# Performance work log

Hardware: AMD Instinct MI355X
Metric: run time of the kernel (lower is better)

## Reference

```python
import jax, jax.numpy as jnp
import numpy as np

E = 1024      # embed_dim
H = 16        # num_heads
D = E // H    # head_dim
SCALING = float(D * 1.0) ** (-0.5)


def setup_inputs() -> dict:
    key = jax.random.key(0)
    ks = jax.random.split(key, 10)
    B, L, S = 4, 2048, 2048
    query = jax.random.normal(ks[0], (B, L, E), dtype=jnp.float32)
    k_in = jax.random.normal(ks[1], (B, S, E), dtype=jnp.float32)
    v_in = jax.random.normal(ks[2], (B, S, E), dtype=jnp.float32)
    attn_bias = jax.random.normal(ks[3], (L, S), dtype=jnp.float32)
    attn_mask = jax.random.normal(ks[4], (L, S), dtype=jnp.float32)
    # in_proj: Linear(E, 3E)  (xavier-uniform-ish scale), out_proj: Linear(E, E)
    lim_in = np.sqrt(6.0 / (E + 3 * E))
    Wqkv = jax.random.uniform(ks[5], (3 * E, E), minval=-lim_in, maxval=lim_in, dtype=jnp.float32)
    bqkv = jnp.zeros((3 * E,), dtype=jnp.float32)
    lim_out = np.sqrt(1.0 / E)
    Wo = jax.random.uniform(ks[6], (E, E), minval=-lim_out, maxval=lim_out, dtype=jnp.float32)
    bo = jnp.zeros((E,), dtype=jnp.float32)
    return {"query": query, "key": k_in, "value": v_in,
            "attn_bias": attn_bias, "attn_mask": attn_mask,
            "Wqkv": Wqkv, "bqkv": bqkv, "Wo": Wo, "bo": bo}


def reference(query, key, value, attn_bias, attn_mask, Wqkv, bqkv, Wo, bo):
    B, L, _ = query.shape
    S = key.shape[1]
    # fused in_proj split into q/k/v slices (q from query, k from key, v from value)
    q = query @ Wqkv[:E].T + bqkv[:E]
    k = key @ Wqkv[E:2 * E].T + bqkv[E:2 * E]
    v = value @ Wqkv[2 * E:].T + bqkv[2 * E:]
    q = q * SCALING
    # [B, L, H, D]
    q = q.reshape(B, L, H, D)
    k = k.reshape(B, S, H, D)
    v = v.reshape(B, S, H, D)
    # scores: [B, H, L, S] with additive float mask and bias (broadcast over B, H)
    scores = jnp.einsum("blhd,bshd->bhls", q, k)
    scores = scores + attn_mask[None, None] + attn_bias[None, None]
    weights = jax.nn.softmax(scores, axis=-1)  # dropout p=0.0 -> identity
    out = jnp.einsum("bhls,bshd->blhd", weights, v).reshape(B, L, E)
    return out @ Wo.T + bo
```

## Files before the change

kernel.cpp:

```cpp
#include <hip/hip_runtime.h>
#include <hip/hip_bf16.h>

#define BB 4
#define LL 2048
#define SS 2048
#define EE 1024
#define HH 16
#define DD 64
#define MM (BB * LL)
#define LOG2E 1.44269504088896340736f

typedef unsigned short u16;
typedef u16   u16x4  __attribute__((ext_vector_type(4)));
typedef u16   u16x8  __attribute__((ext_vector_type(8)));
typedef float f32x4  __attribute__((ext_vector_type(4)));
typedef __bf16 bf16x4 __attribute__((ext_vector_type(4)));
typedef __bf16 bf16x8 __attribute__((ext_vector_type(8)));

__device__ __forceinline__ u16 f2bf(float x) {
    unsigned u = __float_as_uint(x);
    u += 0x7fffu + ((u >> 16) & 1u);
    return (u16)(u >> 16);
}
__device__ __forceinline__ float bf2f(u16 b) {
    return __uint_as_float(((unsigned)b) << 16);
}

__device__ __forceinline__ void gload16(const u16* g, u16* l) {
    __builtin_amdgcn_global_load_lds(
        (const __attribute__((address_space(1))) void*)g,
        (__attribute__((address_space(3))) void*)l, 16, 0, 0);
}

__global__ __launch_bounds__(256) void f32_to_bf16_kernel(
    const float* __restrict__ in, u16* __restrict__ out)
{
    size_t idx = ((size_t)blockIdx.x * 256 + threadIdx.x) * 8;
    f32x4 a = *(const f32x4*)(in + idx);
    f32x4 b = *(const f32x4*)(in + idx + 4);
    u16x8 o;
#pragma unroll
    for (int j = 0; j < 4; j++) { o[j] = f2bf(a[j]); o[4 + j] = f2bf(b[j]); }
    *(u16x8*)(out + idx) = o;
}

__global__ __launch_bounds__(256) void combine_bias_kernel(
    const float* __restrict__ bias, const float* __restrict__ mask,
    u16* __restrict__ comb)
{
    int idx = (blockIdx.x * 256 + threadIdx.x) * 8;
    f32x4 a0 = *(const f32x4*)(bias + idx);
    f32x4 a1 = *(const f32x4*)(bias + idx + 4);
    f32x4 m0 = *(const f32x4*)(mask + idx);
    f32x4 m1 = *(const f32x4*)(mask + idx + 4);
    u16x8 o;
#pragma unroll
    for (int j = 0; j < 4; j++) {
        o[j]     = f2bf((a0[j] + m0[j]) * LOG2E);
        o[4 + j] = f2bf((a1[j] + m1[j]) * LOG2E);
    }
    *(u16x8*)(comb + idx) = o;
}

template <int ABF16, int OUTBF16, int VOUT>
__global__ __launch_bounds__(256, 2) void gemm_bt(
    const void* __restrict__ Ap, const u16* __restrict__ Bw,
    const float* __restrict__ bias, void* __restrict__ Cp,
    int M, int N, int K, float scale)
{
    __shared__ __align__(16) u16 SH[128 * 72 + 128 * 64];
    constexpr int ASTR = ABF16 ? 64 : 72;
    u16* As = SH;
    u16* Bs = SH + 128 * ASTR;
    u16* Tr = SH;

    const int tid = threadIdx.x;
    const int lane = tid & 63, wave = tid >> 6;
    const int quad = lane >> 4, ln = lane & 15;
    const int wm = (wave & 1) * 64, wn = (wave >> 1) * 64;

    const int bid = blockIdx.x;
    const int vid = (bid & 7) * 8 + ((bid >> 3) & 7) + (bid >> 6) * 64;
    const int m0 = (vid >> 3) * 128, n0 = (vid & 7) * 128;

    const int r8 = lane >> 3, c8 = lane & 7;
    const float* Af = (const float*)Ap;
    const u16*   Ab = (const u16*)Ap + (size_t)m0 * K + c8 * 8;
    const u16*   Bg = Bw + (size_t)n0 * K + c8 * 8;

    f32x4 acc[4][4];
#pragma unroll
    for (int mt = 0; mt < 4; mt++)
#pragma unroll
        for (int nt = 0; nt < 4; nt++) acc[mt][nt] = (f32x4){0.f, 0.f, 0.f, 0.f};

    f32x4 apf[8];

    auto load_a = [&](int k0) {
        if (!ABF16) {
#pragma unroll
            for (int i = 0; i < 8; i++) {
                int chunk = tid + 256 * i, row = chunk >> 4, c = chunk & 15;
                apf[i] = *(const f32x4*)(Af + (size_t)(m0 + row) * K + k0 + c * 4);
            }
        }
    };

    load_a(0);

    const int KT = K >> 6;
    for (int kt = 0; kt < KT; kt++) {
        const int k0 = kt << 6;
        __syncthreads();
#pragma unroll
        for (int i = 0; i < 4; i++) {
            int ch = i * 4 + wave;
            int row = ch * 8 + r8;
            gload16(Bg + (size_t)row * K + k0, &Bs[ch * 512]);
            if (ABF16) gload16(Ab + (size_t)row * K + k0, &As[ch * 512]);
        }
        if (!ABF16) {
#pragma unroll
            for (int i = 0; i < 8; i++) {
                int chunk = tid + 256 * i, row = chunk >> 4, c = chunk & 15;
                u16x4 o;
#pragma unroll
                for (int j = 0; j < 4; j++) o[j] = f2bf(apf[i][j]);
                *(u16x4*)(As + row * ASTR + c * 4) = o;
            }
        }
        __syncthreads();

        if (kt + 1 < KT) load_a(k0 + 64);

#pragma unroll
        for (int ks = 0; ks < 2; ks++) {
            bf16x8 af[4], bfg[4];
#pragma unroll
            for (int mt = 0; mt < 4; mt++)
                af[mt] = *(const bf16x8*)(&As[(wm + mt * 16 + ln) * ASTR + ks * 32 + quad * 8]);
#pragma unroll
            for (int nt = 0; nt < 4; nt++)
                bfg[nt] = *(const bf16x8*)(&Bs[(wn + nt * 16 + ln) * 64 + ks * 32 + quad * 8]);
#pragma unroll
            for (int mt = 0; mt < 4; mt++)
#pragma unroll
                for (int nt = 0; nt < 4; nt++)
                    acc[mt][nt] = __builtin_amdgcn_mfma_f32_16x16x32_bf16(
                        af[mt], bfg[nt], acc[mt][nt], 0, 0, 0);
        }
    }

    if (VOUT) {
        __syncthreads();
#pragma unroll
        for (int nt = 0; nt < 4; nt++) {
            int nl = wn + nt * 16 + ln;
            float bn = bias[n0 + nl];
#pragma unroll
            for (int mt = 0; mt < 4; mt++)
#pragma unroll
                for (int r = 0; r < 4; r++) {
                    int ml = wm + mt * 16 + quad * 4 + r;
                    Tr[nl * 136 + ml] = f2bf(acc[mt][nt][r] + bn);
                }
        }
        __syncthreads();
        const int bq = m0 >> 11;
        const int s0 = m0 & 2047;
#pragma unroll
        for (int i = 0; i < 8; i++) {
            int chunk = tid + 256 * i;
            int row = chunk >> 4, c = chunk & 15;
            u16x8 v = *(const u16x8*)(Tr + row * 136 + c * 8);
            int n = n0 + row;
            int h = n >> 6, d = n & 63;
            *(u16x8*)(((u16*)Cp) + ((size_t)((bq * 16 + h) * 64 + d)) * SS + s0 + c * 8) = v;
        }
    } else {
#pragma unroll
        for (int nt = 0; nt < 4; nt++) {
            int n = n0 + wn + nt * 16 + ln;
            float bn = bias[n];
#pragma unroll
            for (int mt = 0; mt < 4; mt++) {
#pragma unroll
                for (int r = 0; r < 4; r++) {
                    int m = m0 + wm + mt * 16 + quad * 4 + r;
                    float val = (acc[mt][nt][r] + bn) * scale;
                    if (OUTBF16) ((u16*)Cp)[(size_t)m * N + n] = f2bf(val);
                    else         ((float*)Cp)[(size_t)m * N + n] = val;
                }
            }
        }
    }
}

__global__ __launch_bounds__(256, 2) void attn_kernel(
    const u16* __restrict__ qb,
    const u16* __restrict__ kb,
    const u16* __restrict__ vt,
    const u16* __restrict__ comb,
    u16* __restrict__ attn)
{
    __shared__ __align__(16) u16 KPs[128 * 136];
    __shared__ __align__(16) u16 Vs[64 * 136];
    const int tid = threadIdx.x, lane = tid & 63, wave = tid >> 6;
    const int quad = lane >> 4, ln = lane & 15;

    const int bid = blockIdx.x;
    const int vid = (bid & 7) * 128 + (bid >> 3);
    const int bh = vid >> 4, b = bh >> 4, h = bh & 15;
    const int q0 = (vid & 15) * 128;
    const int qloc0 = wave * 32;

    bf16x8 qf[2][2];
#pragma unroll
    for (int qg = 0; qg < 2; qg++)
#pragma unroll
        for (int ks = 0; ks < 2; ks++)
            qf[qg][ks] = *(const bf16x8*)(qb + (size_t)(b * LL + q0 + qloc0 + 16 * qg + ln) * EE
                                          + h * 64 + ks * 32 + quad * 8);

    const u16* cb0 = comb + (size_t)(q0 + qloc0 + ln) * SS + quad * 4;
    const u16* cb1 = cb0 + (size_t)16 * SS;

    f32x4 o[4][2];
#pragma unroll
    for (int mt = 0; mt < 4; mt++) { o[mt][0] = (f32x4){0,0,0,0}; o[mt][1] = (f32x4){0,0,0,0}; }
    f32x4 ls0 = (f32x4){0,0,0,0}, ls1 = (f32x4){0,0,0,0};

    u16x8 kreg[4], vreg[4];
    auto load_kv = [&](int s0) {
#pragma unroll
        for (int i = 0; i < 4; i++) {
            int chunk = tid + 256 * i, row = chunk >> 3, c = chunk & 7;
            kreg[i] = *(const u16x8*)(kb + (size_t)(b * SS + s0 + row) * EE + h * 64 + c * 8);
        }
#pragma unroll
        for (int i = 0; i < 4; i++) {
            int chunk = tid + 256 * i, row = chunk >> 4, c = chunk & 15;
            vreg[i] = *(const u16x8*)(vt + (size_t)(bh * 64 + row) * SS + s0 + c * 8);
        }
    };
    load_kv(0);

    for (int s0 = 0; s0 < SS; s0 += 128) {
        __syncthreads();
#pragma unroll
        for (int i = 0; i < 4; i++) {
            int chunk = tid + 256 * i, row = chunk >> 3, c = chunk & 7;
            *(u16x8*)(KPs + row * 72 + c * 8) = kreg[i];
        }
#pragma unroll
        for (int i = 0; i < 4; i++) {
            int chunk = tid + 256 * i, row = chunk >> 4, c = chunk & 15;
            *(u16x8*)(Vs + row * 136 + c * 8) = vreg[i];
        }
        u16x4 bfr[8][2];
#pragma unroll
        for (int mt = 0; mt < 8; mt++) {
            bfr[mt][0] = *(const u16x4*)(cb0 + s0 + mt * 16);
            bfr[mt][1] = *(const u16x4*)(cb1 + s0 + mt * 16);
        }
        __syncthreads();

        if (s0 + 128 < SS) load_kv(s0 + 128);

        f32x4 st[8][2];
#pragma unroll
        for (int mt = 0; mt < 8; mt++)
#pragma unroll
            for (int r = 0; r < 4; r++) {
                st[mt][0][r] = bf2f(bfr[mt][0][r]);
                st[mt][1][r] = bf2f(bfr[mt][1][r]);
            }

        __builtin_amdgcn_s_setprio(1);
#pragma unroll
        for (int mt = 0; mt < 8; mt++) {
            bf16x8 a0 = *(const bf16x8*)(KPs + (mt * 16 + ln) * 72 + quad * 8);
            bf16x8 a1 = *(const bf16x8*)(KPs + (mt * 16 + ln) * 72 + 32 + quad * 8);
            st[mt][0] = __builtin_amdgcn_mfma_f32_16x16x32_bf16(a0, qf[0][0], st[mt][0], 0, 0, 0);
            st[mt][0] = __builtin_amdgcn_mfma_f32_16x16x32_bf16(a1, qf[0][1], st[mt][0], 0, 0, 0);
            st[mt][1] = __builtin_amdgcn_mfma_f32_16x16x32_bf16(a0, qf[1][0], st[mt][1], 0, 0, 0);
            st[mt][1] = __builtin_amdgcn_mfma_f32_16x16x32_bf16(a1, qf[1][1], st[mt][1], 0, 0, 0);
        }
        __builtin_amdgcn_s_setprio(0);

        bf16x4 p[8][2];
#pragma unroll
        for (int mt = 0; mt < 8; mt++)
#pragma unroll
            for (int r = 0; r < 4; r++) {
                float e0 = __builtin_amdgcn_exp2f(st[mt][0][r]);
                float e1 = __builtin_amdgcn_exp2f(st[mt][1][r]);
                ls0[r] += e0; ls1[r] += e1;
                p[mt][0][r] = (__bf16)e0;
                p[mt][1][r] = (__bf16)e1;
            }

        __syncthreads();

#pragma unroll
        for (int mt = 0; mt < 8; mt++) {
            *(bf16x4*)(KPs + (qloc0 + ln) * 136 + mt * 16 + quad * 4)      = p[mt][0];
            *(bf16x4*)(KPs + (qloc0 + 16 + ln) * 136 + mt * 16 + quad * 4) = p[mt][1];
        }

#pragma unroll
        for (int ks = 0; ks < 4; ks++) {
            bf16x8 pf0 = *(const bf16x8*)(KPs + (qloc0 + ln) * 136 + ks * 32 + quad * 8);
            bf16x8 pf1 = *(const bf16x8*)(KPs + (qloc0 + 16 + ln) * 136 + ks * 32 + quad * 8);
            __builtin_amdgcn_s_setprio(1);
#pragma unroll
            for (int mt = 0; mt < 4; mt++) {
                bf16x8 a = *(const bf16x8*)(Vs + (mt * 16 + ln) * 136 + ks * 32 + quad * 8);
                o[mt][0] = __builtin_amdgcn_mfma_f32_16x16x32_bf16(a, pf0, o[mt][0], 0, 0, 0);
                o[mt][1] = __builtin_amdgcn_mfma_f32_16x16x32_bf16(a, pf1, o[mt][1], 0, 0, 0);
            }
            __builtin_amdgcn_s_setprio(0);
        }
    }

    float lsum0 = (ls0[0] + ls0[1]) + (ls0[2] + ls0[3]);
    float lsum1 = (ls1[0] + ls1[1]) + (ls1[2] + ls1[3]);
    lsum0 += __shfl_xor(lsum0, 16); lsum0 += __shfl_xor(lsum0, 32);
    lsum1 += __shfl_xor(lsum1, 16); lsum1 += __shfl_xor(lsum1, 32);
    float inv0 = 1.f / lsum0, inv1 = 1.f / lsum1;

#pragma unroll
    for (int mt = 0; mt < 4; mt++) {
        bf16x4 p0, p1;
#pragma unroll
        for (int r = 0; r < 4; r++) {
            p0[r] = (__bf16)(o[mt][0][r] * inv0);
            p1[r] = (__bf16)(o[mt][1][r] * inv1);
        }
        *(bf16x4*)(KPs + (qloc0 + ln) * 136 + mt * 16 + quad * 4)      = p0;
        *(bf16x4*)(KPs + (qloc0 + 16 + ln) * 136 + mt * 16 + quad * 4) = p1;
    }
#pragma unroll
    for (int i = 0; i < 4; i++) {
        int j = lane + 64 * i;
        int r = j >> 3, c = j & 7;
        u16x8 v = *(const u16x8*)(KPs + (qloc0 + r) * 136 + c * 8);
        *(u16x8*)(attn + (size_t)(b * LL + q0 + qloc0 + r) * EE + h * 64 + c * 8) = v;
    }
}

extern "C" void kernel_launch(void* const* d_in, const int* in_sizes, int n_in,
                              void* d_out, int out_size, void* d_ws, size_t ws_size,
                              hipStream_t stream)
{
    (void)in_sizes; (void)n_in; (void)out_size; (void)ws_size;
    const float* query     = (const float*)d_in[0];
    const float* key       = (const float*)d_in[1];
    const float* value     = (const float*)d_in[2];
    const float* attn_bias = (const float*)d_in[3];
    const float* attn_mask = (const float*)d_in[4];
    const float* Wqkv      = (const float*)d_in[5];
    const float* bqkv      = (const float*)d_in[6];
    const float* Wo        = (const float*)d_in[7];
    const float* bo        = (const float*)d_in[8];
    float* out = (float*)d_out;

    u16* wq_bf = (u16*)d_ws;
    u16* wo_bf = wq_bf + 3 * EE * EE;
    u16* comb  = wo_bf + EE * EE;
    u16* q_bf  = comb + (size_t)LL * SS;
    u16* k_bf  = q_bf + (size_t)MM * EE;
    u16* v_bf  = k_bf + (size_t)MM * EE;
    u16* vtr   = v_bf + (size_t)MM * EE;
    u16* attnb = vtr  + (size_t)MM * EE;

    f32_to_bf16_kernel<<<3 * EE * EE / 2048, 256, 0, stream>>>(Wqkv, wq_bf);
    f32_to_bf16_kernel<<<EE * EE / 2048, 256, 0, stream>>>(Wo, wo_bf);
    combine_bias_kernel<<<(LL * SS) / 2048, 256, 0, stream>>>(attn_bias, attn_mask, comb);

    gemm_bt<0, 1, 0><<<512, 256, 0, stream>>>(query, wq_bf,               bqkv,          q_bf, MM, EE, EE, 0.125f * LOG2E);
    gemm_bt<0, 1, 0><<<512, 256, 0, stream>>>(key,   wq_bf + EE * EE,     bqkv + EE,     k_bf, MM, EE, EE, 1.f);
    gemm_bt<0, 1, 1><<<512, 256, 0, stream>>>(value, wq_bf + 2 * EE * EE, bqkv + 2 * EE, vtr,  MM, EE, EE, 1.f);

    attn_kernel<<<1024, 256, 0, stream>>>(q_bf, k_bf, vtr, comb, attnb);

    gemm_bt<1, 0, 0><<<512, 256, 0, stream>>>(attnb, wo_bf, bo, out, MM, EE, EE, 1.f);
}
```

Measured before the change: 434.1 us.

## Double-buffer GEMM shared tiles and split attention QK work by key columns per wave

```diff
diff --git a/kernel.cpp b/kernel.cpp
--- a/kernel.cpp
+++ b/kernel.cpp
@@ -68,11 +68,11 @@
     const float* __restrict__ bias, void* __restrict__ Cp,
     int M, int N, int K, float scale)
 {
-    __shared__ __align__(16) u16 SH[128 * 72 + 128 * 64];
+    __shared__ __align__(16) u16 SH[ABF16 ? (4 * 128 * 64) : (128 * 72 + 2 * 128 * 64)];
     constexpr int ASTR = ABF16 ? 64 : 72;
-    u16* As = SH;
-    u16* Bs = SH + 128 * ASTR;
-    u16* Tr = SH;
+    u16* As  = SH;
+    u16* Bs  = SH + (ABF16 ? 2 * 128 * 64 : 128 * 72);
+    u16* Tr  = SH;
 
     const int tid = threadIdx.x;
     const int lane = tid & 63, wave = tid >> 6;
@@ -105,20 +105,32 @@
             }
         }
     };
+    auto stage_b = [&](int bu, int k0) {
+#pragma unroll
+        for (int i = 0; i < 4; i++) {
+            int ch = i * 4 + wave;
+            int row = ch * 8 + r8;
+            gload16(Bg + (size_t)row * K + k0, &Bs[bu * (128 * 64) + ch * 512]);
+        }
+    };
+    auto stage_a16 = [&](int bu, int k0) {
+#pragma unroll
+        for (int i = 0; i < 4; i++) {
+            int ch = i * 4 + wave;
+            int row = ch * 8 + r8;
+            gload16(Ab + (size_t)row * K + k0, &As[bu * (128 * 64) + ch * 512]);
+        }
+    };
 
     load_a(0);
-
+    stage_b(0, 0);
+    if (ABF16) stage_a16(0, 0);
+
+    int buf = 0;
     const int KT = K >> 6;
     for (int kt = 0; kt < KT; kt++) {
         const int k0 = kt << 6;
         __syncthreads();
-#pragma unroll
-        for (int i = 0; i < 4; i++) {
-            int ch = i * 4 + wave;
-            int row = ch * 8 + r8;
-            gload16(Bg + (size_t)row * K + k0, &Bs[ch * 512]);
-            if (ABF16) gload16(Ab + (size_t)row * K + k0, &As[ch * 512]);
-        }
         if (!ABF16) {
 #pragma unroll
             for (int i = 0; i < 8; i++) {
@@ -128,20 +140,25 @@
                 for (int j = 0; j < 4; j++) o[j] = f2bf(apf[i][j]);
                 *(u16x4*)(As + row * ASTR + c * 4) = o;
             }
-        }
-        __syncthreads();
-
-        if (kt + 1 < KT) load_a(k0 + 64);
-
+            __syncthreads();
+        }
+        if (kt + 1 < KT) {
+            stage_b(buf ^ 1, k0 + 64);
+            if (ABF16) stage_a16(buf ^ 1, k0 + 64);
+            load_a(k0 + 64);
+        }
+
+        const u16* Ar = ABF16 ? &As[buf * (128 * 64)] : As;
+        const u16* Br = &Bs[buf * (128 * 64)];
 #pragma unroll
         for (int ks = 0; ks < 2; ks++) {
             bf16x8 af[4], bfg[4];
 #pragma unroll
             for (int mt = 0; mt < 4; mt++)
-                af[mt] = *(const bf16x8*)(&As[(wm + mt * 16 + ln) * ASTR + ks * 32 + quad * 8]);
+                af[mt] = *(const bf16x8*)(&Ar[(wm + mt * 16 + ln) * ASTR + ks * 32 + quad * 8]);
 #pragma unroll
             for (int nt = 0; nt < 4; nt++)
-                bfg[nt] = *(const bf16x8*)(&Bs[(wn + nt * 16 + ln) * 64 + ks * 32 + quad * 8]);
+                bfg[nt] = *(const bf16x8*)(&Br[(wn + nt * 16 + ln) * 64 + ks * 32 + quad * 8]);
 #pragma unroll
             for (int mt = 0; mt < 4; mt++)
 #pragma unroll
@@ -149,6 +166,7 @@
                     acc[mt][nt] = __builtin_amdgcn_mfma_f32_16x16x32_bf16(
                         af[mt], bfg[nt], acc[mt][nt], 0, 0, 0);
         }
+        buf ^= 1;
     }
 
     if (VOUT) {
@@ -214,21 +232,22 @@
     const int q0 = (vid & 15) * 128;
     const int qloc0 = wave * 32;
 
-    bf16x8 qf[2][2];
-#pragma unroll
-    for (int qg = 0; qg < 2; qg++)
+    bf16x8 qf[8][2];
+#pragma unroll
+    for (int qg = 0; qg < 8; qg++)
 #pragma unroll
         for (int ks = 0; ks < 2; ks++)
-            qf[qg][ks] = *(const bf16x8*)(qb + (size_t)(b * LL + q0 + qloc0 + 16 * qg + ln) * EE
+            qf[qg][ks] = *(const bf16x8*)(qb + (size_t)(b * LL + q0 + qg * 16 + ln) * EE
                                           + h * 64 + ks * 32 + quad * 8);
 
-    const u16* cb0 = comb + (size_t)(q0 + qloc0 + ln) * SS + quad * 4;
-    const u16* cb1 = cb0 + (size_t)16 * SS;
+    const u16* cbase = comb + (size_t)(q0 + ln) * SS + wave * 32 + quad * 4;
 
     f32x4 o[4][2];
 #pragma unroll
     for (int mt = 0; mt < 4; mt++) { o[mt][0] = (f32x4){0,0,0,0}; o[mt][1] = (f32x4){0,0,0,0}; }
-    f32x4 ls0 = (f32x4){0,0,0,0}, ls1 = (f32x4){0,0,0,0};
+    float ls[8];
+#pragma unroll
+    for (int qg = 0; qg < 8; qg++) ls[qg] = 0.f;
 
     u16x8 kreg[4], vreg[4];
     auto load_kv = [&](int s0) {
@@ -257,56 +276,60 @@
             int chunk = tid + 256 * i, row = chunk >> 4, c = chunk & 15;
             *(u16x8*)(Vs + row * 136 + c * 8) = vreg[i];
         }
-        u16x4 bfr[8][2];
-#pragma unroll
-        for (int mt = 0; mt < 8; mt++) {
-            bfr[mt][0] = *(const u16x4*)(cb0 + s0 + mt * 16);
-            bfr[mt][1] = *(const u16x4*)(cb1 + s0 + mt * 16);
-        }
+        u16x4 bfr[2][8];
+#pragma unroll
+        for (int m = 0; m < 2; m++)
+#pragma unroll
+            for (int qg = 0; qg < 8; qg++)
+                bfr[m][qg] = *(const u16x4*)(cbase + (size_t)qg * 16 * SS + s0 + m * 16);
         __syncthreads();
 
         if (s0 + 128 < SS) load_kv(s0 + 128);
 
-        f32x4 st[8][2];
-#pragma unroll
-        for (int mt = 0; mt < 8; mt++)
-#pragma unroll
-            for (int r = 0; r < 4; r++) {
-                st[mt][0][r] = bf2f(bfr[mt][0][r]);
-                st[mt][1][r] = bf2f(bfr[mt][1][r]);
+        f32x4 st[2][8];
+#pragma unroll
+        for (int m = 0; m < 2; m++)
+#pragma unroll
+            for (int qg = 0; qg < 8; qg++)
+#pragma unroll
+                for (int r = 0; r < 4; r++)
+                    st[m][qg][r] = bf2f(bfr[m][qg][r]);
+
+        __builtin_amdgcn_s_setprio(1);
+#pragma unroll
+        for (int m = 0; m < 2; m++) {
+            const int row = (wave * 2 + m) * 16 + ln;
+            bf16x8 a0 = *(const bf16x8*)(KPs + row * 72 + quad * 8);
+            bf16x8 a1 = *(const bf16x8*)(KPs + row * 72 + 32 + quad * 8);
+#pragma unroll
+            for (int qg = 0; qg < 8; qg++) {
+                st[m][qg] = __builtin_amdgcn_mfma_f32_16x16x32_bf16(a0, qf[qg][0], st[m][qg], 0, 0, 0);
+                st[m][qg] = __builtin_amdgcn_mfma_f32_16x16x32_bf16(a1, qf[qg][1], st[m][qg], 0, 0, 0);
             }
-
-        __builtin_amdgcn_s_setprio(1);
-#pragma unroll
-        for (int mt = 0; mt < 8; mt++) {
-            bf16x8 a0 = *(const bf16x8*)(KPs + (mt * 16 + ln) * 72 + quad * 8);
-            bf16x8 a1 = *(const bf16x8*)(KPs + (mt * 16 + ln) * 72 + 32 + quad * 8);
-            st[mt][0] = __builtin_amdgcn_mfma_f32_16x16x32_bf16(a0, qf[0][0], st[mt][0], 0, 0, 0);
-            st[mt][0] = __builtin_amdgcn_mfma_f32_16x16x32_bf16(a1, qf[0][1], st[mt][0], 0, 0, 0);
-            st[mt][1] = __builtin_amdgcn_mfma_f32_16x16x32_bf16(a0, qf[1][0], st[mt][1], 0, 0, 0);
-            st[mt][1] = __builtin_amdgcn_mfma_f32_16x16x32_bf16(a1, qf[1][1], st[mt][1], 0, 0, 0);
         }
         __builtin_amdgcn_s_setprio(0);
 
-        bf16x4 p[8][2];
-#pragma unroll
-        for (int mt = 0; mt < 8; mt++)
-#pragma unroll
-            for (int r = 0; r < 4; r++) {
-                float e0 = __builtin_amdgcn_exp2f(st[mt][0][r]);
-                float e1 = __builtin_amdgcn_exp2f(st[mt][1][r]);
-                ls0[r] += e0; ls1[r] += e1;
-                p[mt][0][r] = (__bf16)e0;
-                p[mt][1][r] = (__bf16)e1;
-            }
-
-        __syncthreads();
-
-#pragma unroll
-        for (int mt = 0; mt < 8; mt++) {
-            *(bf16x4*)(KPs + (qloc0 + ln) * 136 + mt * 16 + quad * 4)      = p[mt][0];
-            *(bf16x4*)(KPs + (qloc0 + 16 + ln) * 136 + mt * 16 + quad * 4) = p[mt][1];
-        }
+        bf16x4 p[2][8];
+#pragma unroll
+        for (int m = 0; m < 2; m++)
+#pragma unroll
+            for (int qg = 0; qg < 8; qg++)
+#pragma unroll
+                for (int r = 0; r < 4; r++) {
+                    float e = __builtin_amdgcn_exp2f(st[m][qg][r]);
+                    ls[qg] += e;
+                    p[m][qg][r] = (__bf16)e;
+                }
+
+        __syncthreads();
+
+#pragma unroll
+        for (int m = 0; m < 2; m++)
+#pragma unroll
+            for (int qg = 0; qg < 8; qg++)
+                *(bf16x4*)(KPs + (qg * 16 + ln) * 136 + wave * 32 + m * 16 + quad * 4) = p[m][qg];
+
+        __syncthreads();
 
 #pragma unroll
         for (int ks = 0; ks < 4; ks++) {
@@ -323,10 +346,25 @@
         }
     }
 
-    float lsum0 = (ls0[0] + ls0[1]) + (ls0[2] + ls0[3]);
-    float lsum1 = (ls1[0] + ls1[1]) + (ls1[2] + ls1[3]);
-    lsum0 += __shfl_xor(lsum0, 16); lsum0 += __shfl_xor(lsum0, 32);
-    lsum1 += __shfl_xor(lsum1, 16); lsum1 += __shfl_xor(lsum1, 32);
+#pragma unroll
+    for (int qg = 0; qg < 8; qg++) {
+        ls[qg] += __shfl_xor(ls[qg], 16);
+        ls[qg] += __shfl_xor(ls[qg], 32);
+    }
+    __syncthreads();
+    float* lscr = (float*)Vs;
+    if (lane < 16) {
+#pragma unroll
+        for (int qg = 0; qg < 8; qg++)
+            lscr[wave * 128 + qg * 16 + lane] = ls[qg];
+    }
+    __syncthreads();
+    float lsum0 = 0.f, lsum1 = 0.f;
+#pragma unroll
+    for (int w = 0; w < 4; w++) {
+        lsum0 += lscr[w * 128 + (2 * wave) * 16 + ln];
+        lsum1 += lscr[w * 128 + (2 * wave + 1) * 16 + ln];
+    }
     float inv0 = 1.f / lsum0, inv1 = 1.f / lsum1;
 
 #pragma unroll
```

Measured after the change: 441.1 us. About the same (+1.6%).

## Merge QKV projections into one launch and double-buffer GEMM shared-memory staging

Applied to the files above, without the earlier changes.

```diff
diff --git a/kernel.cpp b/kernel.cpp
--- a/kernel.cpp
+++ b/kernel.cpp
@@ -62,16 +62,15 @@
     *(u16x8*)(comb + idx) = o;
 }
 
-template <int ABF16, int OUTBF16, int VOUT>
-__global__ __launch_bounds__(256, 2) void gemm_bt(
-    const void* __restrict__ Ap, const u16* __restrict__ Bw,
-    const float* __restrict__ bias, void* __restrict__ Cp,
-    int M, int N, int K, float scale)
-{
-    __shared__ __align__(16) u16 SH[128 * 72 + 128 * 64];
-    constexpr int ASTR = ABF16 ? 64 : 72;
+__global__ __launch_bounds__(256, 2) void gemm_qkv(
+    const float* __restrict__ q_in, const float* __restrict__ k_in,
+    const float* __restrict__ v_in, const u16* __restrict__ Wb,
+    const float* __restrict__ bq, u16* __restrict__ q_out,
+    u16* __restrict__ k_out, u16* __restrict__ vtr)
+{
+    __shared__ __align__(16) u16 SH[128 * 72 + 2 * 128 * 64];
     u16* As = SH;
-    u16* Bs = SH + 128 * ASTR;
+    u16* Bs = SH + 128 * 72;
     u16* Tr = SH;
 
     const int tid = threadIdx.x;
@@ -79,14 +78,18 @@
     const int quad = lane >> 4, ln = lane & 15;
     const int wm = (wave & 1) * 64, wn = (wave >> 1) * 64;
 
-    const int bid = blockIdx.x;
+    const int sub = blockIdx.x >> 9;
+    const int bid = blockIdx.x & 511;
     const int vid = (bid & 7) * 8 + ((bid >> 3) & 7) + (bid >> 6) * 64;
     const int m0 = (vid >> 3) * 128, n0 = (vid & 7) * 128;
 
+    const float* Af  = sub == 0 ? q_in : (sub == 1 ? k_in : v_in);
+    const u16*   Bg  = Wb + (size_t)sub * EE * EE + (size_t)n0 * EE;
+    const float* bias = bq + sub * EE;
+    const float scale = (sub == 0) ? 0.125f * LOG2E : 1.f;
+
     const int r8 = lane >> 3, c8 = lane & 7;
-    const float* Af = (const float*)Ap;
-    const u16*   Ab = (const u16*)Ap + (size_t)m0 * K + c8 * 8;
-    const u16*   Bg = Bw + (size_t)n0 * K + c8 * 8;
+    Bg += c8 * 8;
 
     f32x4 acc[4][4];
 #pragma unroll
@@ -97,51 +100,52 @@
     f32x4 apf[8];
 
     auto load_a = [&](int k0) {
-        if (!ABF16) {
-#pragma unroll
-            for (int i = 0; i < 8; i++) {
-                int chunk = tid + 256 * i, row = chunk >> 4, c = chunk & 15;
-                apf[i] = *(const f32x4*)(Af + (size_t)(m0 + row) * K + k0 + c * 4);
-            }
+#pragma unroll
+        for (int i = 0; i < 8; i++) {
+            int chunk = tid + 256 * i, row = chunk >> 4, c = chunk & 15;
+            apf[i] = *(const f32x4*)(Af + (size_t)(m0 + row) * EE + k0 + c * 4);
         }
     };
-
-    load_a(0);
-
-    const int KT = K >> 6;
-    for (int kt = 0; kt < KT; kt++) {
-        const int k0 = kt << 6;
-        __syncthreads();
+    auto stage_b = [&](int bu, int k0) {
 #pragma unroll
         for (int i = 0; i < 4; i++) {
             int ch = i * 4 + wave;
             int row = ch * 8 + r8;
-            gload16(Bg + (size_t)row * K + k0, &Bs[ch * 512]);
-            if (ABF16) gload16(Ab + (size_t)row * K + k0, &As[ch * 512]);
-        }
-        if (!ABF16) {
-#pragma unroll
-            for (int i = 0; i < 8; i++) {
-                int chunk = tid + 256 * i, row = chunk >> 4, c = chunk & 15;
-                u16x4 o;
-#pragma unroll
-                for (int j = 0; j < 4; j++) o[j] = f2bf(apf[i][j]);
-                *(u16x4*)(As + row * ASTR + c * 4) = o;
-            }
-        }
-        __syncthreads();
-
-        if (kt + 1 < KT) load_a(k0 + 64);
-
+            gload16(Bg + (size_t)row * EE + k0, &Bs[bu * (128 * 64) + ch * 512]);
+        }
+    };
+
+    load_a(0);
+    stage_b(0, 0);
+
+    int buf = 0;
+    for (int kt = 0; kt < EE / 64; kt++) {
+        const int k0 = kt << 6;
+        __syncthreads();
+#pragma unroll
+        for (int i = 0; i < 8; i++) {
+            int chunk = tid + 256 * i, row = chunk >> 4, c = chunk & 15;
+            u16x4 o;
+#pragma unroll
+            for (int j = 0; j < 4; j++) o[j] = f2bf(apf[i][j]);
+            *(u16x4*)(As + row * 72 + c * 4) = o;
+        }
+        __syncthreads();
+        if (kt + 1 < EE / 64) {
+            stage_b(buf ^ 1, k0 + 64);
+            load_a(k0 + 64);
+        }
+
+        const u16* Br = &Bs[buf * (128 * 64)];
 #pragma unroll
         for (int ks = 0; ks < 2; ks++) {
             bf16x8 af[4], bfg[4];
 #pragma unroll
             for (int mt = 0; mt < 4; mt++)
-                af[mt] = *(const bf16x8*)(&As[(wm + mt * 16 + ln) * ASTR + ks * 32 + quad * 8]);
+                af[mt] = *(const bf16x8*)(&As[(wm + mt * 16 + ln) * 72 + ks * 32 + quad * 8]);
 #pragma unroll
             for (int nt = 0; nt < 4; nt++)
-                bfg[nt] = *(const bf16x8*)(&Bs[(wn + nt * 16 + ln) * 64 + ks * 32 + quad * 8]);
+                bfg[nt] = *(const bf16x8*)(&Br[(wn + nt * 16 + ln) * 64 + ks * 32 + quad * 8]);
 #pragma unroll
             for (int mt = 0; mt < 4; mt++)
 #pragma unroll
@@ -149,9 +153,10 @@
                     acc[mt][nt] = __builtin_amdgcn_mfma_f32_16x16x32_bf16(
                         af[mt], bfg[nt], acc[mt][nt], 0, 0, 0);
         }
-    }
-
-    if (VOUT) {
+        buf ^= 1;
+    }
+
+    if (sub == 2) {
         __syncthreads();
 #pragma unroll
         for (int nt = 0; nt < 4; nt++) {
@@ -166,7 +171,7 @@
                 }
         }
         __syncthreads();
-        const int bq = m0 >> 11;
+        const int bq_ = m0 >> 11;
         const int s0 = m0 & 2047;
 #pragma unroll
         for (int i = 0; i < 8; i++) {
@@ -175,9 +180,10 @@
             u16x8 v = *(const u16x8*)(Tr + row * 136 + c * 8);
             int n = n0 + row;
             int h = n >> 6, d = n & 63;
-            *(u16x8*)(((u16*)Cp) + ((size_t)((bq * 16 + h) * 64 + d)) * SS + s0 + c * 8) = v;
+            *(u16x8*)(vtr + ((size_t)((bq_ * 16 + h) * 64 + d)) * SS + s0 + c * 8) = v;
         }
     } else {
+        u16* Cp = (sub == 0) ? q_out : k_out;
 #pragma unroll
         for (int nt = 0; nt < 4; nt++) {
             int n = n0 + wn + nt * 16 + ln;
@@ -187,16 +193,94 @@
 #pragma unroll
                 for (int r = 0; r < 4; r++) {
                     int m = m0 + wm + mt * 16 + quad * 4 + r;
-                    float val = (acc[mt][nt][r] + bn) * scale;
-                    if (OUTBF16) ((u16*)Cp)[(size_t)m * N + n] = f2bf(val);
-                    else         ((float*)Cp)[(size_t)m * N + n] = val;
+                    Cp[(size_t)m * EE + n] = f2bf((acc[mt][nt][r] + bn) * scale);
                 }
             }
         }
     }
 }
 
-__global__ __launch_bounds__(256, 2) void attn_kernel(
+__global__ __launch_bounds__(256, 2) void gemm_out(
+    const u16* __restrict__ A, const u16* __restrict__ Bw,
+    const float* __restrict__ bias, float* __restrict__ Cp)
+{
+    __shared__ __align__(16) u16 SH[4 * 128 * 64];
+    u16* As = SH;
+    u16* Bs = SH + 2 * 128 * 64;
+
+    const int tid = threadIdx.x;
+    const int lane = tid & 63, wave = tid >> 6;
+    const int quad = lane >> 4, ln = lane & 15;
+    const int wm = (wave & 1) * 64, wn = (wave >> 1) * 64;
+
+    const int bid = blockIdx.x;
+    const int vid = (bid & 7) * 8 + ((bid >> 3) & 7) + (bid >> 6) * 64;
+    const int m0 = (vid >> 3) * 128, n0 = (vid & 7) * 128;
+
+    const int r8 = lane >> 3, c8 = lane & 7;
+    const u16* Ag = A  + (size_t)m0 * EE + c8 * 8;
+    const u16* Bg = Bw + (size_t)n0 * EE + c8 * 8;
+
+    f32x4 acc[4][4];
+#pragma unroll
+    for (int mt = 0; mt < 4; mt++)
+#pragma unroll
+        for (int nt = 0; nt < 4; nt++) acc[mt][nt] = (f32x4){0.f, 0.f, 0.f, 0.f};
+
+    auto stage = [&](int bu, int k0) {
+#pragma unroll
+        for (int i = 0; i < 4; i++) {
+            int ch = i * 4 + wave;
+            int row = ch * 8 + r8;
+            gload16(Ag + (size_t)row * EE + k0, &As[bu * (128 * 64) + ch * 512]);
+            gload16(Bg + (size_t)row * EE + k0, &Bs[bu * (128 * 64) + ch * 512]);
+        }
+    };
+
+    stage(0, 0);
+    int buf = 0;
+    for (int kt = 0; kt < EE / 64; kt++) {
+        const int k0 = kt << 6;
+        __syncthreads();
+        if (kt + 1 < EE / 64) stage(buf ^ 1, k0 + 64);
+
+        const u16* Ar = &As[buf * (128 * 64)];
+        const u16* Br = &Bs[buf * (128 * 64)];
+#pragma unroll
+        for (int ks = 0; ks < 2; ks++) {
+            bf16x8 af[4], bfg[4];
+#pragma unroll
+            for (int mt = 0; mt < 4; mt++)
+                af[mt] = *(const bf16x8*)(&Ar[(wm + mt * 16 + ln) * 64 + ks * 32 + quad * 8]);
+#pragma unroll
+            for (int nt = 0; nt < 4; nt++)
+                bfg[nt] = *(const bf16x8*)(&Br[(wn + nt * 16 + ln) * 64 + ks * 32 + quad * 8]);
+#pragma unroll
+            for (int mt = 0; mt < 4; mt++)
+#pragma unroll
+                for (int nt = 0; nt < 4; nt++)
+                    acc[mt][nt] = __builtin_amdgcn_mfma_f32_16x16x32_bf16(
+                        af[mt], bfg[nt], acc[mt][nt], 0, 0, 0);
+        }
+        buf ^= 1;
+    }
+
+#pragma unroll
+    for (int nt = 0; nt < 4; nt++) {
+        int n = n0 + wn + nt * 16 + ln;
+        float bn = bias[n];
+#pragma unroll
+        for (int mt = 0; mt < 4; mt++) {
+#pragma unroll
+            for (int r = 0; r < 4; r++) {
+                int m = m0 + wm + mt * 16 + quad * 4 + r;
+                Cp[(size_t)m * EE + n] = acc[mt][nt][r] + bn;
+            }
+        }
+    }
+}
+
+__global__ __launch_bounds__(256, 3) void attn_kernel(
     const u16* __restrict__ qb,
     const u16* __restrict__ kb,
     const u16* __restrict__ vt,
@@ -378,11 +462,10 @@
     f32_to_bf16_kernel<<<EE * EE / 2048, 256, 0, stream>>>(Wo, wo_bf);
     combine_bias_kernel<<<(LL * SS) / 2048, 256, 0, stream>>>(attn_bias, attn_mask, comb);
 
-    gemm_bt<0, 1, 0><<<512, 256, 0, stream>>>(query, wq_bf,               bqkv,          q_bf, MM, EE, EE, 0.125f * LOG2E);
-    gemm_bt<0, 1, 0><<<512, 256, 0, stream>>>(key,   wq_bf + EE * EE,     bqkv + EE,     k_bf, MM, EE, EE, 1.f);
-    gemm_bt<0, 1, 1><<<512, 256, 0, stream>>>(value, wq_bf + 2 * EE * EE, bqkv + 2 * EE, vtr,  MM, EE, EE, 1.f);
+    gemm_qkv<<<1536, 256, 0, stream>>>(query, key, value, wq_bf, bqkv,
+                                       q_bf, k_bf, vtr);
 
     attn_kernel<<<1024, 256, 0, stream>>>(q_bf, k_bf, vtr, comb, attnb);
 
-    gemm_bt<1, 0, 0><<<512, 256, 0, stream>>>(attnb, wo_bf, bo, out, MM, EE, EE, 1.f);
-}
+    gemm_out<<<512, 256, 0, stream>>>(attnb, wo_bf, bo, out);
+}
```

New measurement: 519.6 us. 19.7% more time.
